# Optimization experiments

Measured on AMD Instinct MI355X. Metric: run time of the kernel, lower is better.

Reference implementation:

```python
import jax, jax.numpy as jnp
import numpy as np

B, N, D = 4, 2048, 1024


def setup_inputs() -> dict:
    key = jax.random.key(0)
    ks = jax.random.split(key, 9)
    x = jax.random.normal(ks[0], (B, N, D), dtype=jnp.float32)
    # causal mask: True = masked (set to -inf), per dot_product_attention semantics
    mask = jnp.triu(jnp.ones((N, N), dtype=bool), k=1)
    mask = jnp.broadcast_to(mask, (B, N, N))
    scale = 1.0 / np.sqrt(D)
    Wq = jax.random.normal(ks[1], (D, D), dtype=jnp.float32) * scale
    Wk = jax.random.normal(ks[2], (D, D), dtype=jnp.float32) * scale
    Wv = jax.random.normal(ks[3], (D, D), dtype=jnp.float32) * scale
    Wo = jax.random.normal(ks[4], (D, D), dtype=jnp.float32) * scale
    bq = jnp.zeros((D,), dtype=jnp.float32)
    bk = jnp.zeros((D,), dtype=jnp.float32)
    bv = jnp.zeros((D,), dtype=jnp.float32)
    bo = jnp.zeros((D,), dtype=jnp.float32)
    return {"x": x, "mask": mask, "Wq": Wq, "bq": bq, "Wk": Wk, "bk": bk,
            "Wv": Wv, "bv": bv, "Wo": Wo, "bo": bo}


def reference(x, mask, Wq, bq, Wk, bk, Wv, bv, Wo, bo):
    # QKV projections (single-head despite docstring; module never splits heads)
    Q = x @ Wq + bq  # [b, n, d]
    K = x @ Wk + bk
    V = x @ Wv + bv
    d = K.shape[-1]
    scores = jnp.einsum('bqd,bkd->bqk', Q, K) / jnp.sqrt(jnp.asarray(d, Q.dtype))
    min_infty = jnp.finfo(scores.dtype).min
    scores = jnp.where(mask, min_infty, scores)
    weights = jax.nn.softmax(scores, axis=-1)
    attention = jnp.einsum('bqk,bkd->bqd', weights, V)
    out = attention @ Wo + bo
    return out
```

## Files before the change

kernel.cpp:

```cpp
#include <hip/hip_runtime.h>
#include <hip/hip_bf16.h>

typedef __attribute__((ext_vector_type(8))) short short8;
typedef __attribute__((ext_vector_type(4))) float f32x4;

__device__ inline float b2f(unsigned short u) {
    union { unsigned int i; float f; } c; c.i = ((unsigned int)u) << 16; return c.f;
}
__device__ inline unsigned short f2b(float f) {
    __hip_bfloat16 h = __float2bfloat16(f);
    return *reinterpret_cast<unsigned short*>(&h);
}

__device__ inline void gl_lds16(const unsigned short* g, unsigned short* ldsbase) {
    __builtin_amdgcn_global_load_lds(
        (const __attribute__((address_space(1))) unsigned int*)(g),
        (__attribute__((address_space(3))) unsigned int*)(ldsbase),
        16, 0, 0);
}

__global__ __launch_bounds__(256) void prep(
    const float* __restrict__ x,
    const float* __restrict__ Wq, const float* __restrict__ Wk,
    const float* __restrict__ Wo, const float* __restrict__ Wv,
    const float* __restrict__ bv, const float* __restrict__ bo,
    unsigned short* __restrict__ xb,
    unsigned short* __restrict__ Wqt, unsigned short* __restrict__ Wkt,
    unsigned short* __restrict__ Wot, unsigned short* __restrict__ Wvb,
    float* __restrict__ bvo)
{
    const int z = blockIdx.z;
    const int t = threadIdx.x;
    __shared__ float tile[32][33];

    if (z < 3) {
        const float* src = z == 0 ? Wq : z == 1 ? Wk : Wo;
        unsigned short* dst = z == 0 ? Wqt : z == 1 ? Wkt : Wot;
        const int c0 = blockIdx.x * 32, r0 = blockIdx.y * 32;
        const int tx = t & 31, ty = t >> 5;
        #pragma unroll
        for (int i = ty; i < 32; i += 8)
            tile[i][tx] = src[(long)(r0 + i) * 1024 + c0 + tx];
        __syncthreads();
        #pragma unroll
        for (int i = ty; i < 32; i += 8)
            dst[(long)(c0 + i) * 1024 + r0 + tx] = f2b(tile[tx][i]);
        return;
    }
    if (z == 3) {
        const int i = (blockIdx.y * 32 + blockIdx.x) * 256 + t;
        float4 v = ((const float4*)Wv)[i];
        union { unsigned short u[4]; unsigned long long ll; } p;
        p.u[0] = f2b(v.x); p.u[1] = f2b(v.y); p.u[2] = f2b(v.z); p.u[3] = f2b(v.w);
        ((unsigned long long*)Wvb)[i] = p.ll;
        return;
    }
    if (z < 6) {
        const int bl = (z - 4) * 1024 + blockIdx.y * 32 + blockIdx.x;
        #pragma unroll
        for (int k = 0; k < 4; k++) {
            const int i = bl * 1024 + k * 256 + t;
            float4 v = ((const float4*)x)[i];
            union { unsigned short u[4]; unsigned long long ll; } p;
            p.u[0] = f2b(v.x); p.u[1] = f2b(v.y); p.u[2] = f2b(v.z); p.u[3] = f2b(v.w);
            ((unsigned long long*)xb)[i] = p.ll;
        }
        return;
    }
    if (blockIdx.y != 0) return;
    const int tx = t & 31, ty = t >> 5;
    const int n = blockIdx.x * 32 + tx;
    float acc = 0.f;
    #pragma unroll 4
    for (int j = 0; j < 128; j++) {
        const int k = ty * 128 + j;
        acc += Wo[(long)k * 1024 + n] * bv[k];
    }
    float* red = &tile[0][0];
    red[ty * 32 + tx] = acc;
    __syncthreads();
    if (ty == 0) {
        float s = 0.f;
        #pragma unroll
        for (int j = 0; j < 8; j++) s += red[j * 32 + tx];
        bvo[n] = s + bo[n];
    }
}

#define TILE_KLOOP(As, Bs, gA, lda, gB, ldb, Keff) \
    for (int k0 = 0; k0 < (Keff); k0 += 64) { \
        _Pragma("unroll") for (int p = 0; p < 2; p++) \
            _Pragma("unroll") for (int h = 0; h < 2; h++) { \
                gl_lds16((gA) + (long)h * 16 * (lda) + k0 + p * 32, \
                         &(As)[p * 4096 + (w * 32 + h * 16) * 32]); \
                gl_lds16((gB) + (long)h * 16 * (ldb) + k0 + p * 32, \
                         &(Bs)[p * 4096 + (w * 32 + h * 16) * 32]); \
            } \
        __syncthreads(); \
        _Pragma("unroll") for (int p = 0; p < 2; p++) { \
            short8 af[4], bfr[4]; \
            _Pragma("unroll") for (int mi = 0; mi < 4; mi++) \
                af[mi] = *(const short8*)&(As)[p * 4096 + (wr * 64 + mi * 16 + lrow) * 32 + quad * 8]; \
            _Pragma("unroll") for (int ni = 0; ni < 4; ni++) \
                bfr[ni] = *(const short8*)&(Bs)[p * 4096 + (wc * 64 + ni * 16 + lrow) * 32 + quad * 8]; \
            _Pragma("unroll") for (int mi = 0; mi < 4; mi++) \
                _Pragma("unroll") for (int ni = 0; ni < 4; ni++) \
                    acc[mi][ni] = __builtin_amdgcn_mfma_f32_16x16x32_bf16( \
                        af[mi], bfr[ni], acc[mi][ni], 0, 0, 0); \
        } \
        __syncthreads(); \
    }

#define TILE_DECLS \
    const int t = threadIdx.x, lane = t & 63, w = t >> 6; \
    const int wr = w >> 1, wc = w & 1; \
    const int lrow = lane & 15, quad = lane >> 4; \
    f32x4 acc[4][4]; \
    _Pragma("unroll") for (int i = 0; i < 4; i++) \
        _Pragma("unroll") for (int j = 0; j < 4; j++) \
            acc[i][j] = (f32x4){0.f, 0.f, 0.f, 0.f};

__global__ __launch_bounds__(256) void gemm128(
    const unsigned short* __restrict__ A, const unsigned short* __restrict__ Bt,
    unsigned short* __restrict__ C)
{
    __shared__ __attribute__((aligned(16))) unsigned short As[2 * 128 * 32];
    __shared__ __attribute__((aligned(16))) unsigned short Bs[2 * 128 * 32];
    const int m0 = blockIdx.x * 128, n0 = blockIdx.y * 128;

    TILE_DECLS

    const unsigned short* gA = A  + (long)(m0 + w * 32 + (lane >> 2)) * 1024 + (lane & 3) * 8;
    const unsigned short* gB = Bt + (long)(n0 + w * 32 + (lane >> 2)) * 1024 + (lane & 3) * 8;
    TILE_KLOOP(As, Bs, gA, 1024, gB, 1024, 1024)

    #pragma unroll
    for (int mi = 0; mi < 4; mi++) {
        const int m = m0 + wr * 64 + mi * 16 + quad * 4;
        #pragma unroll
        for (int ni = 0; ni < 4; ni++) {
            const int n = n0 + wc * 64 + ni * 16 + lrow;
            #pragma unroll
            for (int rg = 0; rg < 4; rg++)
                C[(long)(m + rg) * 1024 + n] = f2b(acc[mi][ni][rg]);
        }
    }
}

#define TILE2_DECLS \
    const int t = threadIdx.x, lane = t & 63, w = t >> 6; \
    const int wr = w >> 1, wc = w & 1; \
    const int lrow = lane & 15, quad = lane >> 4; \
    f32x4 acc0[4][4], acc1[4][4]; \
    _Pragma("unroll") for (int i = 0; i < 4; i++) \
        _Pragma("unroll") for (int j = 0; j < 4; j++) { \
            acc0[i][j] = (f32x4){0.f, 0.f, 0.f, 0.f}; \
            acc1[i][j] = (f32x4){0.f, 0.f, 0.f, 0.f}; \
        }

#define TILE2_KLOOP(gA, lda, gB0, gB1, ldb, Keff) \
    for (int k0 = 0; k0 < (Keff); k0 += 64) { \
        _Pragma("unroll") for (int p = 0; p < 2; p++) \
            _Pragma("unroll") for (int h = 0; h < 2; h++) { \
                const int ldst = p * 4096 + (w * 32 + h * 16) * 32; \
                const long gofs = (long)h * 16 * (lda) + k0 + p * 32; \
                const long gofsB = (long)h * 16 * (ldb) + k0 + p * 32; \
                gl_lds16((gA)  + gofs,  &As[ldst]); \
                gl_lds16((gB0) + gofsB, &Bs0[ldst]); \
                gl_lds16((gB1) + gofsB, &Bs1[ldst]); \
            } \
        __syncthreads(); \
        _Pragma("unroll") for (int p = 0; p < 2; p++) { \
            short8 af[4], bfr[4]; \
            _Pragma("unroll") for (int mi = 0; mi < 4; mi++) \
                af[mi] = *(const short8*)&As[p * 4096 + (wr * 64 + mi * 16 + lrow) * 32 + quad * 8]; \
            _Pragma("unroll") for (int ni = 0; ni < 4; ni++) \
                bfr[ni] = *(const short8*)&Bs0[p * 4096 + (wc * 64 + ni * 16 + lrow) * 32 + quad * 8]; \
            _Pragma("unroll") for (int mi = 0; mi < 4; mi++) \
                _Pragma("unroll") for (int ni = 0; ni < 4; ni++) \
                    acc0[mi][ni] = __builtin_amdgcn_mfma_f32_16x16x32_bf16( \
                        af[mi], bfr[ni], acc0[mi][ni], 0, 0, 0); \
            _Pragma("unroll") for (int ni = 0; ni < 4; ni++) \
                bfr[ni] = *(const short8*)&Bs1[p * 4096 + (wc * 64 + ni * 16 + lrow) * 32 + quad * 8]; \
            _Pragma("unroll") for (int mi = 0; mi < 4; mi++) \
                _Pragma("unroll") for (int ni = 0; ni < 4; ni++) \
                    acc1[mi][ni] = __builtin_amdgcn_mfma_f32_16x16x32_bf16( \
                        af[mi], bfr[ni], acc1[mi][ni], 0, 0, 0); \
        } \
        __syncthreads(); \
    }

__global__ __launch_bounds__(256, 2) void gemm_qk2(
    const unsigned short* __restrict__ Q, const unsigned short* __restrict__ Km,
    unsigned short* __restrict__ S)
{
    __shared__ __attribute__((aligned(16))) unsigned short As[8192];
    __shared__ __attribute__((aligned(16))) unsigned short Bs0[8192];
    __shared__ __attribute__((aligned(16))) unsigned short Bs1[8192];

    const int q = 71 - blockIdx.x;
    int tq = (int)sqrtf((float)q);
    while (tq * tq + tq > q) tq--;
    while ((tq + 1) * (tq + 1) + (tq + 1) <= q) tq++;
    int bm, bp;
    if (q >= (tq + 1) * (tq + 1)) { bm = 2 * tq + 1; bp = q - (tq + 1) * (tq + 1); }
    else                          { bm = 2 * tq;     bp = q - (tq * tq + tq); }
    const int bz = blockIdx.y;
    const unsigned short* A  = Q  + (long)bz * 2048 * 1024;
    const unsigned short* Bt = Km + (long)bz * 2048 * 1024;
    const int m0 = bm * 128, n0 = bp * 256;

    TILE2_DECLS

    const unsigned short* gA  = A  + (long)(m0 + w * 32 + (lane >> 2)) * 1024 + (lane & 3) * 8;
    const unsigned short* gB0 = Bt + (long)(n0 + w * 32 + (lane >> 2)) * 1024 + (lane & 3) * 8;
    const unsigned short* gB1 = gB0 + 128L * 1024;
    TILE2_KLOOP(gA, 1024, gB0, gB1, 1024, 1024)

    unsigned short* Sb = S + (long)bz * 2048 * 2048;
    #pragma unroll
    for (int mi = 0; mi < 4; mi++) {
        const int m = m0 + wr * 64 + mi * 16 + quad * 4;
        #pragma unroll
        for (int ni = 0; ni < 4; ni++) {
            const int nl = wc * 64 + ni * 16 + lrow;
            #pragma unroll
            for (int rg = 0; rg < 4; rg++) {
                Sb[(long)(m + rg) * 2048 + n0 + nl]       = f2b(acc0[mi][ni][rg] * 0.03125f);
                Sb[(long)(m + rg) * 2048 + n0 + 128 + nl] = f2b(acc1[mi][ni][rg] * 0.03125f);
            }
        }
    }
}

__global__ __launch_bounds__(256, 2) void gemm_pv2(
    const unsigned short* __restrict__ S, const unsigned short* __restrict__ Vot,
    const float* __restrict__ bvo, float* __restrict__ out)
{
    __shared__ __attribute__((aligned(16))) unsigned short As[8192];
    __shared__ __attribute__((aligned(16))) unsigned short Bs0[8192];
    __shared__ __attribute__((aligned(16))) unsigned short Bs1[8192];

    const int bm = 15 - (int)blockIdx.x;
    const int bn2 = blockIdx.y, bz = blockIdx.z;
    const unsigned short* A  = S   + (long)bz * 2048 * 2048;
    const unsigned short* Bt = Vot + (long)bz * 2048;
    const int m0 = bm * 128, n0 = bn2 * 256;
    const int Keff = (bm + 1) * 128;

    TILE2_DECLS

    const unsigned short* gA  = A  + (long)(m0 + w * 32 + (lane >> 2)) * 2048 + (lane & 3) * 8;
    const unsigned short* gB0 = Bt + (long)(n0 + w * 32 + (lane >> 2)) * 8192 + (lane & 3) * 8;
    const unsigned short* gB1 = gB0 + 128L * 8192;
    TILE2_KLOOP(gA, 2048, gB0, gB1, 8192, Keff)

    float* ob = out + (long)bz * 2048 * 1024;
    #pragma unroll
    for (int mi = 0; mi < 4; mi++) {
        const int m = m0 + wr * 64 + mi * 16 + quad * 4;
        #pragma unroll
        for (int ni = 0; ni < 4; ni++) {
            const int nl = wc * 64 + ni * 16 + lrow;
            const float bv0 = bvo[n0 + nl];
            const float bv1 = bvo[n0 + 128 + nl];
            #pragma unroll
            for (int rg = 0; rg < 4; rg++) {
                ob[(long)(m + rg) * 1024 + n0 + nl]       = acc0[mi][ni][rg] + bv0;
                ob[(long)(m + rg) * 1024 + n0 + 128 + nl] = acc1[mi][ni][rg] + bv1;
            }
        }
    }
}

__global__ __launch_bounds__(256, 2) void qkv_proj(
    const unsigned short* __restrict__ A,
    const unsigned short* __restrict__ Wqt, const unsigned short* __restrict__ Wkt,
    const unsigned short* __restrict__ Wvot,
    const float* __restrict__ bq, const float* __restrict__ bk,
    unsigned short* __restrict__ Q, unsigned short* __restrict__ Km,
    unsigned short* __restrict__ Vot)
{
    __shared__ __attribute__((aligned(16))) unsigned short smem[32768];
    unsigned short* As  = smem;
    unsigned short* Bs0 = smem + 8192;
    unsigned short* Bs1 = smem + 16384;
    unsigned short* Bs2 = smem + 24576;
    unsigned short* pool = smem;

    const int bid = blockIdx.x;
    const int bnn = bid & 7, bm = bid >> 3;
    const int m0 = bm * 128, n0 = bnn * 128;

    const int t = threadIdx.x, lane = t & 63, w = t >> 6;
    const int wr = w >> 1, wc = w & 1;
    const int lrow = lane & 15, quad = lane >> 4;

    f32x4 accQ[4][4], accK[4][4], accV[4][4];
    #pragma unroll
    for (int i = 0; i < 4; i++)
        #pragma unroll
        for (int j = 0; j < 4; j++) {
            accQ[i][j] = (f32x4){0.f, 0.f, 0.f, 0.f};
            accK[i][j] = (f32x4){0.f, 0.f, 0.f, 0.f};
            accV[i][j] = (f32x4){0.f, 0.f, 0.f, 0.f};
        }

    const long rowA = (long)(m0 + w * 32 + (lane >> 2)) * 1024 + (lane & 3) * 8;
    const long rowB = (long)(n0 + w * 32 + (lane >> 2)) * 1024 + (lane & 3) * 8;
    const unsigned short* gA  = A    + rowA;
    const unsigned short* gB0 = Wqt  + rowB;
    const unsigned short* gB1 = Wkt  + rowB;
    const unsigned short* gB2 = Wvot + rowB;

    for (int k0 = 0; k0 < 1024; k0 += 64) {
        #pragma unroll
        for (int p = 0; p < 2; p++)
            #pragma unroll
            for (int h = 0; h < 2; h++) {
                const int ldst = p * 4096 + (w * 32 + h * 16) * 32;
                const long gofs = (long)h * 16 * 1024 + k0 + p * 32;
                gl_lds16(gA  + gofs, &As[ldst]);
                gl_lds16(gB0 + gofs, &Bs0[ldst]);
                gl_lds16(gB1 + gofs, &Bs1[ldst]);
                gl_lds16(gB2 + gofs, &Bs2[ldst]);
            }
        __syncthreads();
        #pragma unroll
        for (int p = 0; p < 2; p++) {
            short8 af[4], bfr[4];
            #pragma unroll
            for (int mi = 0; mi < 4; mi++)
                af[mi] = *(const short8*)&As[p * 4096 + (wr * 64 + mi * 16 + lrow) * 32 + quad * 8];
            #pragma unroll
            for (int ni = 0; ni < 4; ni++)
                bfr[ni] = *(const short8*)&Bs0[p * 4096 + (wc * 64 + ni * 16 + lrow) * 32 + quad * 8];
            #pragma unroll
            for (int mi = 0; mi < 4; mi++)
                #pragma unroll
                for (int ni = 0; ni < 4; ni++)
                    accQ[mi][ni] = __builtin_amdgcn_mfma_f32_16x16x32_bf16(
                        af[mi], bfr[ni], accQ[mi][ni], 0, 0, 0);
            #pragma unroll
            for (int ni = 0; ni < 4; ni++)
                bfr[ni] = *(const short8*)&Bs1[p * 4096 + (wc * 64 + ni * 16 + lrow) * 32 + quad * 8];
            #pragma unroll
            for (int mi = 0; mi < 4; mi++)
                #pragma unroll
                for (int ni = 0; ni < 4; ni++)
                    accK[mi][ni] = __builtin_amdgcn_mfma_f32_16x16x32_bf16(
                        af[mi], bfr[ni], accK[mi][ni], 0, 0, 0);
            #pragma unroll
            for (int ni = 0; ni < 4; ni++)
                bfr[ni] = *(const short8*)&Bs2[p * 4096 + (wc * 64 + ni * 16 + lrow) * 32 + quad * 8];
            #pragma unroll
            for (int mi = 0; mi < 4; mi++)
                #pragma unroll
                for (int ni = 0; ni < 4; ni++)
                    accV[mi][ni] = __builtin_amdgcn_mfma_f32_16x16x32_bf16(
                        af[mi], bfr[ni], accV[mi][ni], 0, 0, 0);
        }
        __syncthreads();
    }

    #pragma unroll
    for (int mi = 0; mi < 4; mi++)
        #pragma unroll
        for (int ni = 0; ni < 4; ni++) {
            const int n_l = wc * 64 + ni * 16 + lrow;
            const float bvl = bq[n0 + n_l];
            #pragma unroll
            for (int rg = 0; rg < 4; rg++) {
                const int m_l = wr * 64 + mi * 16 + quad * 4 + rg;
                pool[m_l * 128 + n_l] = f2b(accQ[mi][ni][rg] + bvl);
            }
        }
    __syncthreads();
    #pragma unroll
    for (int it = 0; it < 8; it++) {
        const int idx = it * 256 + t;
        const int m_l = idx >> 4, c = idx & 15;
        short8 v = *(const short8*)&pool[m_l * 128 + c * 8];
        *(short8*)&Q[(long)(m0 + m_l) * 1024 + n0 + c * 8] = v;
    }
    __syncthreads();

    #pragma unroll
    for (int mi = 0; mi < 4; mi++)
        #pragma unroll
        for (int ni = 0; ni < 4; ni++) {
            const int n_l = wc * 64 + ni * 16 + lrow;
            const float bvl = bk[n0 + n_l];
            #pragma unroll
            for (int rg = 0; rg < 4; rg++) {
                const int m_l = wr * 64 + mi * 16 + quad * 4 + rg;
                pool[m_l * 128 + n_l] = f2b(accK[mi][ni][rg] + bvl);
            }
        }
    __syncthreads();
    #pragma unroll
    for (int it = 0; it < 8; it++) {
        const int idx = it * 256 + t;
        const int m_l = idx >> 4, c = idx & 15;
        short8 v = *(const short8*)&pool[m_l * 128 + c * 8];
        *(short8*)&Km[(long)(m0 + m_l) * 1024 + n0 + c * 8] = v;
    }
    __syncthreads();

    #pragma unroll
    for (int mi = 0; mi < 4; mi++)
        #pragma unroll
        for (int ni = 0; ni < 4; ni++) {
            const int n_l = wc * 64 + ni * 16 + lrow;
            const int mb = wr * 64 + mi * 16 + quad * 4;
            union { unsigned short u[4]; unsigned long long ll; } pk;
            #pragma unroll
            for (int rg = 0; rg < 4; rg++) pk.u[rg] = f2b(accV[mi][ni][rg]);
            *(unsigned long long*)&pool[n_l * 128 + (mb ^ ((n_l & 15) << 3))] = pk.ll;
        }
    __syncthreads();
    #pragma unroll
    for (int it = 0; it < 8; it++) {
        const int idx = it * 256 + t;
        const int n_l = idx >> 4, c = idx & 15;
        short8 v = *(const short8*)&pool[n_l * 128 + ((c * 8) ^ ((n_l & 15) << 3))];
        *(short8*)&Vot[(long)(n0 + n_l) * 8192 + m0 + c * 8] = v;
    }
}

__global__ __launch_bounds__(256) void softmax_causal(unsigned short* __restrict__ S)
{
    const int i = blockIdx.x;
    const int t = threadIdx.x;
    const int padded = ((i >> 7) + 1) << 7;
    const int j0 = t * 8;
    const bool active = j0 < padded;

    __shared__ float red[4];

    for (int b = 0; b < 4; b++) {
        unsigned short* base = S + ((long)b * 2048 + i) * 2048;

        float v[8];
        if (active) {
            short8 s8 = *(const short8*)(base + j0);
            #pragma unroll
            for (int jj = 0; jj < 8; jj++)
                v[jj] = (j0 + jj <= i) ? b2f((unsigned short)s8[jj]) : -3.0e38f;
        } else {
            #pragma unroll
            for (int jj = 0; jj < 8; jj++) v[jj] = -3.0e38f;
        }

        float lmax = v[0];
        #pragma unroll
        for (int jj = 1; jj < 8; jj++) lmax = fmaxf(lmax, v[jj]);
        #pragma unroll
        for (int off = 32; off > 0; off >>= 1) lmax = fmaxf(lmax, __shfl_xor(lmax, off, 64));
        if ((t & 63) == 0) red[t >> 6] = lmax;
        __syncthreads();
        const float gmax = fmaxf(fmaxf(red[0], red[1]), fmaxf(red[2], red[3]));
        __syncthreads();

        float lsum = 0.f;
        #pragma unroll
        for (int jj = 0; jj < 8; jj++) {
            v[jj] = (v[jj] > -1.0e37f) ? __expf(v[jj] - gmax) : 0.f;
            lsum += v[jj];
        }
        #pragma unroll
        for (int off = 32; off > 0; off >>= 1) lsum += __shfl_xor(lsum, off, 64);
        if ((t & 63) == 0) red[t >> 6] = lsum;
        __syncthreads();
        const float inv = 1.0f / (red[0] + red[1] + red[2] + red[3]);

        if (active) {
            short8 p8;
            #pragma unroll
            for (int jj = 0; jj < 8; jj++) p8[jj] = (short)f2b(v[jj] * inv);
            *(short8*)(base + j0) = p8;
        }
        __syncthreads();
    }
}

extern "C" void kernel_launch(void* const* d_in, const int* in_sizes, int n_in,
                              void* d_out, int out_size, void* d_ws, size_t ws_size,
                              hipStream_t stream)
{
    const float* x  = (const float*)d_in[0];
    const float* Wq = (const float*)d_in[2];
    const float* bq = (const float*)d_in[3];
    const float* Wk = (const float*)d_in[4];
    const float* bk = (const float*)d_in[5];
    const float* Wv = (const float*)d_in[6];
    const float* bv = (const float*)d_in[7];
    const float* Wo = (const float*)d_in[8];
    const float* bo = (const float*)d_in[9];

    unsigned short* ws = (unsigned short*)d_ws;
    const long XSZ = 8192L * 1024;
    const long WSZ = 1024L * 1024;
    unsigned short* xb   = ws;
    unsigned short* Wqt  = ws + XSZ;
    unsigned short* Wkt  = Wqt + WSZ;
    unsigned short* Wot  = Wkt + WSZ;
    unsigned short* Wvb  = Wot + WSZ;
    unsigned short* Wvot = Wvb + WSZ;
    unsigned short* Q    = Wvot + WSZ;
    unsigned short* Km   = Q + XSZ;
    unsigned short* Vot  = Km + XSZ;
    unsigned short* S    = Vot + XSZ;
    float*          bvo  = (float*)(S + 4L * 2048 * 2048);

    const dim3 blk(256);

    prep<<<dim3(32, 32, 7), blk, 0, stream>>>(
        x, Wq, Wk, Wo, Wv, bv, bo, xb, Wqt, Wkt, Wot, Wvb, bvo);

    gemm128<<<dim3(8, 8), blk, 0, stream>>>(Wot, Wvb, Wvot);

    qkv_proj<<<dim3(512), blk, 0, stream>>>(
        xb, Wqt, Wkt, Wvot, bq, bk, Q, Km, Vot);

    gemm_qk2<<<dim3(72, 4), blk, 0, stream>>>(Q, Km, S);

    softmax_causal<<<dim3(2048), blk, 0, stream>>>(S);

    gemm_pv2<<<dim3(16, 4, 4), blk, 0, stream>>>(S, Vot, bvo, (float*)d_out);
}
```

Measured before the change: 326.9 us.

## Shrink PV GEMM tile to 128x64 for more blocks and occupancy

Replaces the 128x256-tile PV GEMM with a simpler 128x64-tile kernel that uses less LDS and fewer accumulators, allowing four blocks per CU. The grid grows from 256 to 1024 blocks, which is meant to balance the triangular causal workload across the GPU's many CUs. In exchange, each block re-reads the same S rows for every 64-column output slice, so A-operand traffic rises, and the K loop loses the double-buffered pipelining the old macro may have had.

```diff
diff --git a/kernel.cpp b/kernel.cpp
--- a/kernel.cpp
+++ b/kernel.cpp
@@ -233,42 +233,74 @@
     }
 }
 
-__global__ __launch_bounds__(256, 2) void gemm_pv2(
+__global__ __launch_bounds__(256, 4) void gemm_pv1(
     const unsigned short* __restrict__ S, const unsigned short* __restrict__ Vot,
     const float* __restrict__ bvo, float* __restrict__ out)
 {
     __shared__ __attribute__((aligned(16))) unsigned short As[8192];
-    __shared__ __attribute__((aligned(16))) unsigned short Bs0[8192];
-    __shared__ __attribute__((aligned(16))) unsigned short Bs1[8192];
-
-    const int bm = 15 - (int)blockIdx.x;
-    const int bn2 = blockIdx.y, bz = blockIdx.z;
+    __shared__ __attribute__((aligned(16))) unsigned short Bs[4096];
+
+    const int bn = blockIdx.x;
+    const int bm = 15 - (int)blockIdx.y;
+    const int bz = blockIdx.z;
     const unsigned short* A  = S   + (long)bz * 2048 * 2048;
     const unsigned short* Bt = Vot + (long)bz * 2048;
-    const int m0 = bm * 128, n0 = bn2 * 256;
+    const int m0 = bm * 128, n0 = bn * 64;
     const int Keff = (bm + 1) * 128;
 
-    TILE2_DECLS
-
-    const unsigned short* gA  = A  + (long)(m0 + w * 32 + (lane >> 2)) * 2048 + (lane & 3) * 8;
-    const unsigned short* gB0 = Bt + (long)(n0 + w * 32 + (lane >> 2)) * 8192 + (lane & 3) * 8;
-    const unsigned short* gB1 = gB0 + 128L * 8192;
-    TILE2_KLOOP(gA, 2048, gB0, gB1, 8192, Keff)
+    const int t = threadIdx.x, lane = t & 63, w = t >> 6;
+    const int lrow = lane & 15, quad = lane >> 4;
+
+    f32x4 acc[2][4];
+    #pragma unroll
+    for (int i = 0; i < 2; i++)
+        #pragma unroll
+        for (int j = 0; j < 4; j++)
+            acc[i][j] = (f32x4){0.f, 0.f, 0.f, 0.f};
+
+    const unsigned short* gA = A  + (long)(m0 + w * 32 + (lane >> 2)) * 2048 + (lane & 3) * 8;
+    const unsigned short* gB = Bt + (long)(n0 + w * 16 + (lane >> 2)) * 8192 + (lane & 3) * 8;
+
+    for (int k0 = 0; k0 < Keff; k0 += 64) {
+        #pragma unroll
+        for (int p = 0; p < 2; p++) {
+            #pragma unroll
+            for (int h = 0; h < 2; h++)
+                gl_lds16(gA + (long)h * 16 * 2048 + k0 + p * 32,
+                         &As[p * 4096 + (w * 32 + h * 16) * 32]);
+            gl_lds16(gB + k0 + p * 32, &Bs[p * 2048 + (w * 16) * 32]);
+        }
+        __syncthreads();
+        #pragma unroll
+        for (int p = 0; p < 2; p++) {
+            short8 af[2], bfr[4];
+            #pragma unroll
+            for (int mi = 0; mi < 2; mi++)
+                af[mi] = *(const short8*)&As[p * 4096 + (w * 32 + mi * 16 + lrow) * 32 + quad * 8];
+            #pragma unroll
+            for (int ni = 0; ni < 4; ni++)
+                bfr[ni] = *(const short8*)&Bs[p * 2048 + (ni * 16 + lrow) * 32 + quad * 8];
+            #pragma unroll
+            for (int mi = 0; mi < 2; mi++)
+                #pragma unroll
+                for (int ni = 0; ni < 4; ni++)
+                    acc[mi][ni] = __builtin_amdgcn_mfma_f32_16x16x32_bf16(
+                        af[mi], bfr[ni], acc[mi][ni], 0, 0, 0);
+        }
+        __syncthreads();
+    }
 
     float* ob = out + (long)bz * 2048 * 1024;
     #pragma unroll
-    for (int mi = 0; mi < 4; mi++) {
-        const int m = m0 + wr * 64 + mi * 16 + quad * 4;
+    for (int mi = 0; mi < 2; mi++) {
+        const int m = m0 + w * 32 + mi * 16 + quad * 4;
         #pragma unroll
         for (int ni = 0; ni < 4; ni++) {
-            const int nl = wc * 64 + ni * 16 + lrow;
-            const float bv0 = bvo[n0 + nl];
-            const float bv1 = bvo[n0 + 128 + nl];
-            #pragma unroll
-            for (int rg = 0; rg < 4; rg++) {
-                ob[(long)(m + rg) * 1024 + n0 + nl]       = acc0[mi][ni][rg] + bv0;
-                ob[(long)(m + rg) * 1024 + n0 + 128 + nl] = acc1[mi][ni][rg] + bv1;
-            }
+            const int n = n0 + ni * 16 + lrow;
+            const float bvl = bvo[n];
+            #pragma unroll
+            for (int rg = 0; rg < 4; rg++)
+                ob[(long)(m + rg) * 1024 + n] = acc[mi][ni][rg] + bvl;
         }
     }
 }
@@ -527,5 +559,5 @@
 
     softmax_causal<<<dim3(2048), blk, 0, stream>>>(S);
 
-    gemm_pv2<<<dim3(16, 4, 4), blk, 0, stream>>>(S, Vot, bvo, (float*)d_out);
-}
+    gemm_pv1<<<dim3(16, 16, 4), blk, 0, stream>>>(S, Vot, bvo, (float*)d_out);
+}
```

New measurement: 326.6 us. About the same (-0.1%).
